# Optimization experiments

Measured on AMD Instinct MI355X. Metric: run time of the kernel, lower is better.

The kernel has to match this reference:

```python
import jax, jax.numpy as jnp
import numpy as np

N = 1024          # number of proposals
D_APP = 1024      # appearance_feature_dim
D_K = 64          # key_feature_dim
D_G = 64          # geo_feature_dim
NR = 16           # n_relations


def setup_inputs() -> dict:
    key = jax.random.key(0)
    ks = jax.random.split(key, 12)
    s = 0.02
    return {
        "f_a": jax.random.normal(ks[0], (N, D_APP), dtype=jnp.float32),
        "position_embedding": jax.random.uniform(ks[1], (N, N, D_G), dtype=jnp.float32),
        # stacked per-relation params; torch Linear weight layout [out, in]
        "WG_w": jax.random.normal(ks[2], (NR, D_G), dtype=jnp.float32) * s,
        "WG_b": jax.random.normal(ks[3], (NR,), dtype=jnp.float32) * s,
        "WK_w": jax.random.normal(ks[4], (NR, D_K, D_APP), dtype=jnp.float32) * s,
        "WK_b": jax.random.normal(ks[5], (NR, D_K), dtype=jnp.float32) * s,
        "WQ_w": jax.random.normal(ks[6], (NR, D_K, D_APP), dtype=jnp.float32) * s,
        "WQ_b": jax.random.normal(ks[7], (NR, D_K), dtype=jnp.float32) * s,
        "WV_w": jax.random.normal(ks[8], (NR, D_K, D_APP), dtype=jnp.float32) * s,
        "WV_b": jax.random.normal(ks[9], (NR, D_K), dtype=jnp.float32) * s,
    }


def reference(f_a, position_embedding, WG_w, WG_b, WK_w, WK_b, WQ_w, WQ_b, WV_w, WV_b):
    n = f_a.shape[0]
    # geometric gate: relu(Linear(pos_emb)) per relation -> [R, N, N]
    pe = position_embedding.reshape(-1, WG_w.shape[1])  # [N*N, D_G]
    w_g = jax.nn.relu(jnp.einsum('pg,rg->rp', pe, WG_w) + WG_b[:, None])
    w_g = w_g.reshape(WG_w.shape[0], n, n)
    # per-relation K/Q/V projections: [R, N, D_K]
    K = jnp.einsum('nf,rdf->rnd', f_a, WK_w) + WK_b[:, None, :]
    Q = jnp.einsum('nf,rdf->rnd', f_a, WQ_w) + WQ_b[:, None, :]
    V = jnp.einsum('nf,rdf->rnd', f_a, WV_w) + WV_b[:, None, :]
    dk = K.shape[-1]
    # note: row index n comes from K, column index m from Q (as in the torch code)
    scores = jnp.einsum('rnd,rmd->rnm', K, Q) / jnp.sqrt(jnp.asarray(dk, K.dtype))
    w_mn = jnp.log(jnp.clip(w_g, 1e-6)) + scores
    attn = jax.nn.softmax(w_mn, axis=2)  # softmax over m (dim=1 in torch NxN view)
    out = jnp.einsum('rnm,rmd->rnd', attn, V)  # [R, N, D_K]
    R, _, d = out.shape
    concat = jnp.transpose(out, (1, 0, 2)).reshape(n, R * d)  # [N, R*D_K]
    return concat + f_a
```

## Files before the change

kernel.cpp:

```cpp
#include <hip/hip_runtime.h>
#include <hip/hip_bf16.h>
#include <hip/hip_fp16.h>
#include <math.h>

#define NN 1024
#define DAPP 1024
#define DK 64
#define DG 64
#define NR 16

typedef __bf16 bf16x8 __attribute__((ext_vector_type(8)));
typedef _Float16 f16x8 __attribute__((ext_vector_type(8)));
typedef _Float16 f16x4 __attribute__((ext_vector_type(4)));
typedef float f32x4 __attribute__((ext_vector_type(4)));

static constexpr size_t OFF_FAB = 0;
static constexpr size_t OFF_WB  = OFF_FAB + (size_t)NN * DAPP * 2;
static constexpr size_t OFF_KB  = OFF_WB + (size_t)3 * NR * DK * DAPP * 2;
static constexpr size_t OFF_QB  = OFF_KB + (size_t)NR * NN * DK * 2;
static constexpr size_t OFF_V   = OFF_QB + (size_t)NR * NN * DK * 2;
static constexpr size_t OFF_S   = OFF_V + (size_t)NR * NN * DK * 4;
static constexpr size_t OFF_ST  = OFF_S + (size_t)NR * NN * NN * 2;

__global__ __launch_bounds__(256) void cast_kernel(
    const float* __restrict__ fa, const float* __restrict__ wk,
    const float* __restrict__ wq, const float* __restrict__ wv,
    __bf16* __restrict__ fab, __bf16* __restrict__ wb) {
  int i8 = (blockIdx.x * 256 + threadIdx.x) * 8;
  const int M1 = NN * DAPP;
  const float* src;
  __bf16* dst;
  int o;
  if (i8 < M1) {
    src = fa; dst = fab; o = i8;
  } else {
    int j = i8 - M1;
    int p = j >> 20;
    o = j & (M1 - 1);
    src = (p == 0) ? wk : ((p == 1) ? wq : wv);
    dst = wb + ((size_t)p << 20);
  }
  float4 a = *(const float4*)(src + o);
  float4 b = *(const float4*)(src + o + 4);
  bf16x8 v;
  v[0] = (__bf16)a.x; v[1] = (__bf16)a.y; v[2] = (__bf16)a.z; v[3] = (__bf16)a.w;
  v[4] = (__bf16)b.x; v[5] = (__bf16)b.y; v[6] = (__bf16)b.z; v[7] = (__bf16)b.w;
  *(bf16x8*)(dst + o) = v;
}

__global__ __launch_bounds__(256) void kqv_kernel(
    const __bf16* __restrict__ fab, const __bf16* __restrict__ wb,
    const float* __restrict__ kbias, const float* __restrict__ qbias,
    const float* __restrict__ vbias,
    __bf16* __restrict__ Kb, __bf16* __restrict__ Qb, float* __restrict__ V) {
  int wave = blockIdx.x * 4 + (threadIdx.x >> 6);
  int l = threadIdx.x & 63;
  int nt = wave / 96;
  int jt = wave % 96;
  int n0 = nt * 32, j0 = jt * 32;
  int ra = l & 15;
  int ko = (l >> 4) * 8;

  f32x4 acc[2][2] = {};
  for (int k0 = 0; k0 < DAPP; k0 += 32) {
    bf16x8 a0 = *(const bf16x8*)(fab + (size_t)(n0 + ra) * DAPP + k0 + ko);
    bf16x8 a1 = *(const bf16x8*)(fab + (size_t)(n0 + 16 + ra) * DAPP + k0 + ko);
    bf16x8 b0 = *(const bf16x8*)(wb + (size_t)(j0 + ra) * DAPP + k0 + ko);
    bf16x8 b1 = *(const bf16x8*)(wb + (size_t)(j0 + 16 + ra) * DAPP + k0 + ko);
    acc[0][0] = __builtin_amdgcn_mfma_f32_16x16x32_bf16(a0, b0, acc[0][0], 0, 0, 0);
    acc[0][1] = __builtin_amdgcn_mfma_f32_16x16x32_bf16(a0, b1, acc[0][1], 0, 0, 0);
    acc[1][0] = __builtin_amdgcn_mfma_f32_16x16x32_bf16(a1, b0, acc[1][0], 0, 0, 0);
    acc[1][1] = __builtin_amdgcn_mfma_f32_16x16x32_bf16(a1, b1, acc[1][1], 0, 0, 0);
  }

  #pragma unroll
  for (int i = 0; i < 2; i++) {
    #pragma unroll
    for (int jj = 0; jj < 2; jj++) {
      #pragma unroll
      for (int q = 0; q < 4; q++) {
        int n = n0 + i * 16 + (l >> 4) * 4 + q;
        int col = j0 + jj * 16 + (l & 15);
        int proj = col >> 10;
        int rd = col & 1023;
        int r = rd >> 6, d = rd & 63;
        float v = acc[i][jj][q];
        size_t oidx = ((size_t)r * NN + n) * DK + d;
        if (proj == 0)      Kb[oidx] = (__bf16)(v + kbias[rd]);
        else if (proj == 1) Qb[oidx] = (__bf16)(v + qbias[rd]);
        else                V[oidx] = v + vbias[rd];
      }
    }
  }
}

__global__ __launch_bounds__(256) void gate_score_kernel(
    const float* __restrict__ pe, const float* __restrict__ WGw,
    const float* __restrict__ WGb,
    const __bf16* __restrict__ Kb, const __bf16* __restrict__ Qb,
    _Float16* __restrict__ X) {
  __shared__ alignas(16) _Float16 lg[4][16][17][20];
  int t = threadIdx.x;
  int l = t & 63, w = t >> 6;
  int job = blockIdx.x * 4 + w;
  int nt = job >> 6, mt = job & 63;
  int n0 = nt * 16, m0 = mt * 16;
  int pr = l & 15;
  int kg = (l >> 4) * 8;
  int mq = (l >> 4) << 2;

  bf16x8 wgf[2];
  #pragma unroll
  for (int f = 0; f < 2; f++) {
    const float* wp = WGw + pr * DG + f * 32 + kg;
    float4 a = *(const float4*)wp;
    float4 b = *(const float4*)(wp + 4);
    bf16x8 v;
    v[0] = (__bf16)a.x; v[1] = (__bf16)a.y; v[2] = (__bf16)a.z; v[3] = (__bf16)a.w;
    v[4] = (__bf16)b.x; v[5] = (__bf16)b.y; v[6] = (__bf16)b.z; v[7] = (__bf16)b.w;
    wgf[f] = v;
  }
  float biasr = WGb[pr];

  #pragma unroll 4
  for (int nl = 0; nl < 16; nl++) {
    const float* pp = pe + (((size_t)(n0 + nl) << 10) + m0 + pr) * DG + kg;
    f32x4 acc = {};
    #pragma unroll
    for (int f = 0; f < 2; f++) {
      float4 a = *(const float4*)(pp + f * 32);
      float4 b = *(const float4*)(pp + f * 32 + 4);
      bf16x8 av;
      av[0] = (__bf16)a.x; av[1] = (__bf16)a.y; av[2] = (__bf16)a.z; av[3] = (__bf16)a.w;
      av[4] = (__bf16)b.x; av[5] = (__bf16)b.y; av[6] = (__bf16)b.z; av[7] = (__bf16)b.w;
      acc = __builtin_amdgcn_mfma_f32_16x16x32_bf16(av, wgf[f], acc, 0, 0, 0);
    }
    f16x4 ov;
    #pragma unroll
    for (int q = 0; q < 4; q++)
      ov[q] = (_Float16)__logf(fmaxf(acc[q] + biasr, 1e-6f));
    *(f16x4*)&lg[w][pr][nl][mq] = ov;
  }

  #pragma unroll 4
  for (int r = 0; r < 16; r++) {
    const __bf16* Kr = Kb + (((size_t)r << 10)) * DK;
    const __bf16* Qr = Qb + (((size_t)r << 10)) * DK;
    f32x4 acc = {};
    #pragma unroll
    for (int f = 0; f < 2; f++) {
      bf16x8 qa = *(const bf16x8*)(Qr + (size_t)(m0 + pr) * DK + f * 32 + kg);
      bf16x8 kb = *(const bf16x8*)(Kr + (size_t)(n0 + pr) * DK + f * 32 + kg);
      acc = __builtin_amdgcn_mfma_f32_16x16x32_bf16(qa, kb, acc, 0, 0, 0);
    }
    f16x4 lgv = *(const f16x4*)&lg[w][r][pr][mq];
    f16x4 xv;
    #pragma unroll
    for (int q = 0; q < 4; q++)
      xv[q] = (_Float16)(acc[q] * 0.125f + (float)lgv[q]);
    *(f16x4*)(X + ((size_t)r << 20) + ((size_t)(n0 + pr) << 10) + m0 + mq) = xv;
  }
}

__global__ __launch_bounds__(256) void stats_kernel(
    const _Float16* __restrict__ X, float2* __restrict__ stats) {
  int row = blockIdx.x * 4 + (threadIdx.x >> 6);
  int l = threadIdx.x & 63;
  const f16x8* Sp = (const f16x8*)(X + ((size_t)row << 10) + l * 16);
  f16x8 a = Sp[0], b = Sp[1];
  float v[16];
  float mx = -1e30f;
  #pragma unroll
  for (int i = 0; i < 8; i++) { v[i] = (float)a[i]; v[8 + i] = (float)b[i]; }
  #pragma unroll
  for (int i = 0; i < 16; i++) mx = fmaxf(mx, v[i]);
  #pragma unroll
  for (int off = 32; off >= 1; off >>= 1) mx = fmaxf(mx, __shfl_xor(mx, off, 64));
  float sm = 0.f;
  #pragma unroll
  for (int i = 0; i < 16; i++) sm += __expf(v[i] - mx);
  #pragma unroll
  for (int off = 32; off >= 1; off >>= 1) sm += __shfl_xor(sm, off, 64);
  if (l == 0) stats[row] = make_float2(mx, sm);
}

__global__ __launch_bounds__(256) void pv_kernel(
    const _Float16* __restrict__ S, const float2* __restrict__ stats,
    const float* __restrict__ V, const float* __restrict__ fa,
    float* __restrict__ out) {
  int r = blockIdx.x >> 5;
  int n0 = (blockIdx.x & 31) * 32;
  __shared__ float Pt[64][36];
  __shared__ float Vt[64][68];
  __shared__ float2 st[32];
  int t = threadIdx.x;
  if (t < 32) st[t] = stats[r * NN + n0 + t];

  int d0 = (t & 15) * 4;
  int nl0 = (t >> 4) * 2;
  float acc[2][4] = {};

  for (int m0 = 0; m0 < NN; m0 += 64) {
    __syncthreads();
    {
      int nl = t >> 3;
      int ml = (t & 7) * 8;
      const _Float16* sp = S + ((size_t)r << 20) + ((size_t)(n0 + nl) << 10) + m0 + ml;
      f16x8 sv = *(const f16x8*)sp;
      float mxn = st[nl].x;
      #pragma unroll
      for (int u = 0; u < 8; u++) Pt[ml + u][nl] = __expf((float)sv[u] - mxn);
    }
    {
      int ml = t >> 2;
      int dq = (t & 3) * 16;
      const float* vp = V + ((size_t)r * NN + m0 + ml) * DK + dq;
      #pragma unroll
      for (int u = 0; u < 4; u++) {
        float4 vv = ((const float4*)vp)[u];
        *(float4*)&Vt[ml][dq + u * 4] = vv;
      }
    }
    __syncthreads();
    #pragma unroll 8
    for (int ml = 0; ml < 64; ml++) {
      float a0 = Pt[ml][nl0];
      float a1 = Pt[ml][nl0 + 1];
      float4 vv = *(const float4*)&Vt[ml][d0];
      acc[0][0] += a0 * vv.x; acc[0][1] += a0 * vv.y;
      acc[0][2] += a0 * vv.z; acc[0][3] += a0 * vv.w;
      acc[1][0] += a1 * vv.x; acc[1][1] += a1 * vv.y;
      acc[1][2] += a1 * vv.z; acc[1][3] += a1 * vv.w;
    }
  }

  #pragma unroll
  for (int i = 0; i < 2; i++) {
    int n = n0 + nl0 + i;
    float rs = 1.0f / st[nl0 + i].y;
    int col = r * DK + d0;
    const float4 f = *(const float4*)(fa + (size_t)n * DAPP + col);
    float4 o;
    o.x = acc[i][0] * rs + f.x;
    o.y = acc[i][1] * rs + f.y;
    o.z = acc[i][2] * rs + f.z;
    o.w = acc[i][3] * rs + f.w;
    *(float4*)(out + (size_t)n * DAPP + col) = o;
  }
}

extern "C" void kernel_launch(void* const* d_in, const int* in_sizes, int n_in,
                              void* d_out, int out_size, void* d_ws, size_t ws_size,
                              hipStream_t stream) {
  const float* fa  = (const float*)d_in[0];
  const float* pe  = (const float*)d_in[1];
  const float* WGw = (const float*)d_in[2];
  const float* WGb = (const float*)d_in[3];
  const float* WKw = (const float*)d_in[4];
  const float* WKb = (const float*)d_in[5];
  const float* WQw = (const float*)d_in[6];
  const float* WQb = (const float*)d_in[7];
  const float* WVw = (const float*)d_in[8];
  const float* WVb = (const float*)d_in[9];
  float* out = (float*)d_out;

  char* ws = (char*)d_ws;
  __bf16* fab = (__bf16*)(ws + OFF_FAB);
  __bf16* wb  = (__bf16*)(ws + OFF_WB);
  __bf16* Kb  = (__bf16*)(ws + OFF_KB);
  __bf16* Qb  = (__bf16*)(ws + OFF_QB);
  float*  V   = (float*)(ws + OFF_V);
  _Float16* X = (_Float16*)(ws + OFF_S);
  float2* st  = (float2*)(ws + OFF_ST);

  cast_kernel<<<2048, 256, 0, stream>>>(fa, WKw, WQw, WVw, fab, wb);
  kqv_kernel<<<768, 256, 0, stream>>>(fab, wb, WKb, WQb, WVb, Kb, Qb, V);
  gate_score_kernel<<<1024, 256, 0, stream>>>(pe, WGw, WGb, Kb, Qb, X);
  stats_kernel<<<4096, 256, 0, stream>>>(X, st);
  pv_kernel<<<512, 256, 0, stream>>>(X, st, V, fa, out);
}
```

Before: 515.8 us.

## Rewrite PV stage with bf16 MFMA and transposed bf16 V layout

The kqv kernel now writes V in bf16, transposed to a [R*DK, N] layout, so the PV kernel can load contiguous 8-element fragments. The PV kernel drops its LDS-staged scalar FP32 FMA loop. Each wave now computes a 16x32 output tile with bf16 MFMA, exponentiating the fp16 scores directly in registers. This removes the LDS traffic and the scalar FMA cost of the attention-times-V product, at the cost of lower precision for the probabilities and V. The grid is 512 blocks of 4 waves, and each wave runs a 1024-long K loop.

```diff
diff --git a/kernel.cpp b/kernel.cpp
--- a/kernel.cpp
+++ b/kernel.cpp
@@ -19,7 +19,7 @@
 static constexpr size_t OFF_KB  = OFF_WB + (size_t)3 * NR * DK * DAPP * 2;
 static constexpr size_t OFF_QB  = OFF_KB + (size_t)NR * NN * DK * 2;
 static constexpr size_t OFF_V   = OFF_QB + (size_t)NR * NN * DK * 2;
-static constexpr size_t OFF_S   = OFF_V + (size_t)NR * NN * DK * 4;
+static constexpr size_t OFF_S   = OFF_V + (size_t)NR * NN * DK * 2;
 static constexpr size_t OFF_ST  = OFF_S + (size_t)NR * NN * NN * 2;
 
 __global__ __launch_bounds__(256) void cast_kernel(
@@ -52,7 +52,7 @@
     const __bf16* __restrict__ fab, const __bf16* __restrict__ wb,
     const float* __restrict__ kbias, const float* __restrict__ qbias,
     const float* __restrict__ vbias,
-    __bf16* __restrict__ Kb, __bf16* __restrict__ Qb, float* __restrict__ V) {
+    __bf16* __restrict__ Kb, __bf16* __restrict__ Qb, __bf16* __restrict__ Vt) {
   int wave = blockIdx.x * 4 + (threadIdx.x >> 6);
   int l = threadIdx.x & 63;
   int nt = wave / 96;
@@ -83,12 +83,14 @@
         int col = j0 + jj * 16 + (l & 15);
         int proj = col >> 10;
         int rd = col & 1023;
-        int r = rd >> 6, d = rd & 63;
         float v = acc[i][jj][q];
-        size_t oidx = ((size_t)r * NN + n) * DK + d;
-        if (proj == 0)      Kb[oidx] = (__bf16)(v + kbias[rd]);
-        else if (proj == 1) Qb[oidx] = (__bf16)(v + qbias[rd]);
-        else                V[oidx] = v + vbias[rd];
+        if (proj == 0) {
+          Kb[((size_t)(rd >> 6) * NN + n) * DK + (rd & 63)] = (__bf16)(v + kbias[rd]);
+        } else if (proj == 1) {
+          Qb[((size_t)(rd >> 6) * NN + n) * DK + (rd & 63)] = (__bf16)(v + qbias[rd]);
+        } else {
+          Vt[(size_t)rd * NN + n] = (__bf16)(v + vbias[rd]);
+        }
       }
     }
   }
@@ -185,67 +187,47 @@
 }
 
 __global__ __launch_bounds__(256) void pv_kernel(
-    const _Float16* __restrict__ S, const float2* __restrict__ stats,
-    const float* __restrict__ V, const float* __restrict__ fa,
+    const _Float16* __restrict__ X, const float2* __restrict__ stats,
+    const __bf16* __restrict__ Vt, const float* __restrict__ fa,
     float* __restrict__ out) {
-  int r = blockIdx.x >> 5;
-  int n0 = (blockIdx.x & 31) * 32;
-  __shared__ float Pt[64][36];
-  __shared__ float Vt[64][68];
-  __shared__ float2 st[32];
   int t = threadIdx.x;
-  if (t < 32) st[t] = stats[r * NN + n0 + t];
-
-  int d0 = (t & 15) * 4;
-  int nl0 = (t >> 4) * 2;
-  float acc[2][4] = {};
-
-  for (int m0 = 0; m0 < NN; m0 += 64) {
-    __syncthreads();
-    {
-      int nl = t >> 3;
-      int ml = (t & 7) * 8;
-      const _Float16* sp = S + ((size_t)r << 20) + ((size_t)(n0 + nl) << 10) + m0 + ml;
-      f16x8 sv = *(const f16x8*)sp;
-      float mxn = st[nl].x;
-      #pragma unroll
-      for (int u = 0; u < 8; u++) Pt[ml + u][nl] = __expf((float)sv[u] - mxn);
-    }
-    {
-      int ml = t >> 2;
-      int dq = (t & 3) * 16;
-      const float* vp = V + ((size_t)r * NN + m0 + ml) * DK + dq;
-      #pragma unroll
-      for (int u = 0; u < 4; u++) {
-        float4 vv = ((const float4*)vp)[u];
-        *(float4*)&Vt[ml][dq + u * 4] = vv;
-      }
-    }
-    __syncthreads();
-    #pragma unroll 8
-    for (int ml = 0; ml < 64; ml++) {
-      float a0 = Pt[ml][nl0];
-      float a1 = Pt[ml][nl0 + 1];
-      float4 vv = *(const float4*)&Vt[ml][d0];
-      acc[0][0] += a0 * vv.x; acc[0][1] += a0 * vv.y;
-      acc[0][2] += a0 * vv.z; acc[0][3] += a0 * vv.w;
-      acc[1][0] += a1 * vv.x; acc[1][1] += a1 * vv.y;
-      acc[1][2] += a1 * vv.z; acc[1][3] += a1 * vv.w;
-    }
-  }
-
-  #pragma unroll
-  for (int i = 0; i < 2; i++) {
-    int n = n0 + nl0 + i;
-    float rs = 1.0f / st[nl0 + i].y;
-    int col = r * DK + d0;
-    const float4 f = *(const float4*)(fa + (size_t)n * DAPP + col);
-    float4 o;
-    o.x = acc[i][0] * rs + f.x;
-    o.y = acc[i][1] * rs + f.y;
-    o.z = acc[i][2] * rs + f.z;
-    o.w = acc[i][3] * rs + f.w;
-    *(float4*)(out + (size_t)n * DAPP + col) = o;
+  int l = t & 63, w = t >> 6;
+  int job = blockIdx.x * 4 + w;
+  int dh = job & 1;
+  int jj = job >> 1;
+  int r = jj >> 6;
+  int n0 = (jj & 63) * 16;
+  int pr = l & 15;
+  int kg = (l >> 4) * 8;
+
+  float mxl = stats[r * NN + n0 + pr].x;
+  const _Float16* Xrow = X + ((size_t)r << 20) + ((size_t)(n0 + pr) << 10);
+  const __bf16* V0 = Vt + (size_t)(r * DK + dh * 32) * NN;
+
+  f32x4 acc[2] = {};
+  #pragma unroll 2
+  for (int k0 = 0; k0 < NN; k0 += 32) {
+    f16x8 xv = *(const f16x8*)(Xrow + k0 + kg);
+    bf16x8 pa;
+    #pragma unroll
+    for (int jq = 0; jq < 8; jq++)
+      pa[jq] = (__bf16)__expf(fminf((float)xv[jq] - mxl, 0.0f));
+    #pragma unroll
+    for (int dt = 0; dt < 2; dt++) {
+      bf16x8 vb = *(const bf16x8*)(V0 + (size_t)(dt * 16 + pr) * NN + k0 + kg);
+      acc[dt] = __builtin_amdgcn_mfma_f32_16x16x32_bf16(pa, vb, acc[dt], 0, 0, 0);
+    }
+  }
+
+  #pragma unroll
+  for (int q = 0; q < 4; q++) {
+    int n = n0 + (l >> 4) * 4 + q;
+    float rs = 1.0f / stats[r * NN + n].y;
+    #pragma unroll
+    for (int dt = 0; dt < 2; dt++) {
+      int col = r * DK + dh * 32 + dt * 16 + pr;
+      out[(size_t)n * DAPP + col] = acc[dt][q] * rs + fa[(size_t)n * DAPP + col];
+    }
   }
 }
 
@@ -269,13 +251,13 @@
   __bf16* wb  = (__bf16*)(ws + OFF_WB);
   __bf16* Kb  = (__bf16*)(ws + OFF_KB);
   __bf16* Qb  = (__bf16*)(ws + OFF_QB);
-  float*  V   = (float*)(ws + OFF_V);
+  __bf16* Vt  = (__bf16*)(ws + OFF_V);
   _Float16* X = (_Float16*)(ws + OFF_S);
   float2* st  = (float2*)(ws + OFF_ST);
 
   cast_kernel<<<2048, 256, 0, stream>>>(fa, WKw, WQw, WVw, fab, wb);
-  kqv_kernel<<<768, 256, 0, stream>>>(fab, wb, WKb, WQb, WVb, Kb, Qb, V);
+  kqv_kernel<<<768, 256, 0, stream>>>(fab, wb, WKb, WQb, WVb, Kb, Qb, Vt);
   gate_score_kernel<<<1024, 256, 0, stream>>>(pe, WGw, WGb, Kb, Qb, X);
   stats_kernel<<<4096, 256, 0, stream>>>(X, st);
-  pv_kernel<<<512, 256, 0, stream>>>(X, st, V, fa, out);
-}
+  pv_kernel<<<512, 256, 0, stream>>>(X, st, Vt, fa, out);
+}
```

Measured after the change: 486.4 us. -5.7%, faster.
